# Kernel optimization log

Measured on AMD Instinct MI355X. Metric: run time of the kernel, lower is better.

The kernel has to match this reference:

```python
import jax, jax.numpy as jnp
import numpy as np

N, E, B, D, H, L = 50000, 800000, 16, 64, 128, 2


def _lin(h, w, b):
    return h @ w + b


def _scatter_mean(v, idx, n):
    s = jax.ops.segment_sum(v, idx, num_segments=n)
    c = jax.ops.segment_sum(jnp.ones((v.shape[0],), v.dtype), idx, num_segments=n)
    return s / jnp.maximum(c, 1.0)[:, None]


def setup_inputs() -> dict:
    key = jax.random.key(0)
    ks = iter(jax.random.split(key, 40))

    def p(*shape):
        return jax.random.normal(next(ks), shape, dtype=jnp.float32) * 0.05

    inp = {
        "x": jax.random.normal(next(ks), (N, D), dtype=jnp.float32),
        "edge_attr": jax.random.normal(next(ks), (E, D), dtype=jnp.float32),
        "u": jax.random.normal(next(ks), (B, D), dtype=jnp.float32),
        "e_w1": p(L, 4 * D, H), "e_b1": p(L, H),
        "e_w2": p(L, H, H), "e_b2": p(L, H),
        "e_w3": p(L, H, D), "e_b3": p(L, D),
        "n1_w1": p(L, 2 * D, H), "n1_b1": p(L, H),
        "n1_w2": p(L, H, H), "n1_b2": p(L, H),
        "n2_w1": p(L, D + H + D, H), "n2_b1": p(L, H),
        "n2_w2": p(L, H, D), "n2_b2": p(L, D),
        "g_w1": p(L, 3 * D, H), "g_b1": p(L, H),
        "g_w2": p(L, H, D), "g_b2": p(L, D),
        "edge_index": jax.random.randint(next(ks), (2, E), 0, N, dtype=jnp.int32),
        "batch": jnp.sort(jax.random.randint(next(ks), (N,), 0, B, dtype=jnp.int32)),
    }
    return inp


def _forward(x, edge_attr, u, params, edge_index, batch):
    row, col = edge_index[0], edge_index[1]
    eb = batch[row]  # [E] graph id per edge
    x0, e0, u0 = x, edge_attr, u
    for l in range(L):
        (e_w1, e_b1, e_w2, e_b2, e_w3, e_b3,
         n1_w1, n1_b1, n1_w2, n1_b2,
         n2_w1, n2_b1, n2_w2, n2_b2,
         g_w1, g_b1, g_w2, g_b2) = [pm[l] for pm in params]
        # Edge model: [E, e+2n+u] -> MLP -> [E, D]
        h = jnp.concatenate([x[row], x[col], edge_attr, u[eb]], axis=1)
        h = jax.nn.relu(_lin(h, e_w1, e_b1))
        h = jax.nn.relu(_lin(h, e_w2, e_b2))
        edge_attr = _lin(h, e_w3, e_b3)
        # Node model: gather src node + edge, MLP1, scatter_mean onto dest, MLP2
        se = jnp.concatenate([x[row], edge_attr], axis=1)  # [E, 2D]
        se = _lin(jax.nn.relu(_lin(se, n1_w1, n1_b1)), n1_w2, n1_b2)
        agg = _scatter_mean(se, col, N)  # [N, H]
        xh = jnp.concatenate([x, agg, u[batch]], axis=1)
        x = _lin(jax.nn.relu(_lin(xh, n2_w1, n2_b1)), n2_w2, n2_b2)
        # Global model: per-graph means of updated nodes/edges
        e_agg = _scatter_mean(edge_attr, eb, B)
        n_agg = _scatter_mean(x, batch, B)
        uh = jnp.concatenate([u, n_agg, e_agg], axis=1)
        u = _lin(jax.nn.relu(_lin(uh, g_w1, g_b1)), g_w2, g_b2)
    return x + x0, edge_attr + e0, u + u0


def reference(x, edge_attr, u, e_w1, e_b1, e_w2, e_b2, e_w3, e_b3, n1_w1, n1_b1, n1_w2, n1_b2, n2_w1, n2_b1, n2_w2, n2_b2, g_w1, g_b1, g_w2, g_b2, edge_index, batch):
    params = (e_w1, e_b1, e_w2, e_b2, e_w3, e_b3,
              n1_w1, n1_b1, n1_w2, n1_b2,
              n2_w1, n2_b1, n2_w2, n2_b2,
              g_w1, g_b1, g_w2, g_b2)
    return _forward(x, edge_attr, u, params, edge_index, batch)
```

## Files before the change

kernel.cpp:

```cpp
#include <hip/hip_runtime.h>

#define N_NODES 50000
#define E_EDGES 800000
#define NG 16
#define DD 64
#define HH 128
#define NB_SCAN 49

typedef __attribute__((ext_vector_type(8))) __bf16 bf16x8;
typedef __attribute__((ext_vector_type(4))) float f32x4;
typedef unsigned int uint;
typedef unsigned short ushort;
typedef __attribute__((ext_vector_type(4))) uint uint4v;

#define MFMA16(a,b,c) __builtin_amdgcn_mfma_f32_16x16x32_bf16((a),(b),(c),0,0,0)

__device__ __forceinline__ ushort f2bf(float f){
  uint u = __builtin_bit_cast(uint, f);
  u += 0x7fffu + ((u >> 16) & 1u);
  return (ushort)(u >> 16);
}
__device__ __forceinline__ uint pk2(float a, float b){
  return (uint)f2bf(a) | ((uint)f2bf(b) << 16);
}
__device__ __forceinline__ float bflo(uint u){ return __builtin_bit_cast(float, u << 16); }
__device__ __forceinline__ float bfhi(uint u){ return __builtin_bit_cast(float, u & 0xffff0000u); }

__device__ __forceinline__ bf16x8 ldfrag(const char* base, int row, int byteoff){
  uint4v v = *(const uint4v*)(base + row*256 + (byteoff ^ ((row & 7) << 4)));
  return __builtin_bit_cast(bf16x8, v);
}
__device__ __forceinline__ uint4v ld_chunk(const char* base, int row, int c16){
  return *(const uint4v*)(base + row*256 + ((c16*16) ^ ((row & 7) << 4)));
}
__device__ __forceinline__ void st_h(char* base, int row, int col, float v){
  *(ushort*)(base + row*256 + ((col*2) ^ ((row & 7) << 4))) = f2bf(v);
}
__device__ __forceinline__ void st_chunk(char* base, int row, int c16, uint4v v){
  *(uint4v*)(base + row*256 + ((c16*16) ^ ((row & 7) << 4))) = v;
}
__device__ __forceinline__ void pack16(char* dst, int r, int c16, const float* src){
  float4 lo = *(const float4*)src;
  float4 hi = *(const float4*)(src + 4);
  uint4v v; v.x = pk2(lo.x, lo.y); v.y = pk2(lo.z, lo.w);
  v.z = pk2(hi.x, hi.y); v.w = pk2(hi.z, hi.w);
  st_chunk(dst, r, c16, v);
}

__device__ __forceinline__ void stage_b(char* sB, const ushort* wt,
                                        int Nout, int Ktot, int koff, int t, int stride){
  for (int task = t; task < Nout*16; task += stride){
    int n = task >> 4, c = task & 15;
    uint4v v = *(const uint4v*)(wt + (long)n*Ktot + koff + c*8);
    st_chunk(sB, n, c, v);
  }
}

__device__ __forceinline__ void gemmN4(const char* A, const char* B,
                                       int mw, int nh, int l15, int lhi, f32x4* acc){
  #pragma unroll
  for (int kt = 0; kt < 4; ++kt){
    bf16x8 a = ldfrag(A, mw*16 + l15, kt*64 + lhi*16);
    #pragma unroll
    for (int n = 0; n < 4; ++n){
      bf16x8 bb = ldfrag(B, (nh*4 + n)*16 + l15, kt*64 + lhi*16);
      acc[n] = MFMA16(a, bb, acc[n]);
    }
  }
}
template<bool RELU>
__device__ __forceinline__ void epiN4(char* dst, const f32x4* acc, const float* bias,
                                      int mw, int nh, int l15, int lhi){
  #pragma unroll
  for (int n = 0; n < 4; ++n){
    int col = nh*64 + n*16 + l15;
    float bv = bias[col];
    #pragma unroll
    for (int j = 0; j < 4; ++j){
      int r = mw*16 + lhi*4 + j;
      float v = acc[n][j] + bv;
      if (RELU) v = fmaxf(v, 0.f);
      st_h(dst, r, col, v);
    }
  }
}

template<int NT>
__device__ __forceinline__ void gemm_acc(const char* A, const char* B,
                                         int wv, int l15, int lhi, f32x4* acc){
  #pragma unroll
  for (int kt = 0; kt < 4; ++kt){
    bf16x8 a = ldfrag(A, wv*16 + l15, kt*64 + lhi*16);
    #pragma unroll
    for (int n = 0; n < NT; ++n){
      bf16x8 bb = ldfrag(B, n*16 + l15, kt*64 + lhi*16);
      acc[n] = MFMA16(a, bb, acc[n]);
    }
  }
}
template<int NT, bool RELU>
__device__ __forceinline__ void epi_lds(char* dst, const f32x4* acc, const float* bias,
                                        int wv, int l15, int lhi){
  #pragma unroll
  for (int n = 0; n < NT; ++n){
    float bv = bias[n*16 + l15];
    #pragma unroll
    for (int j = 0; j < 4; ++j){
      int r = wv*16 + lhi*4 + j;
      float v = acc[n][j] + bv;
      if (RELU) v = fmaxf(v, 0.f);
      st_h(dst, r, n*16 + l15, v);
    }
  }
}

__global__ void pack_weights(const float* __restrict__ e1, const float* __restrict__ e2,
                             const float* __restrict__ e3, const float* __restrict__ n11,
                             const float* __restrict__ n12, const float* __restrict__ n21,
                             const float* __restrict__ n22, ushort* __restrict__ out){
  int idx = blockIdx.x * 256 + threadIdx.x;
  int l = idx / 131072, r = idx % 131072;
  const float* src; int K, N, off;
  if      (r <  32768){ src = e1;  K = 256; N = 128; off = 0; }
  else if (r <  49152){ src = e2;  K = 128; N = 128; off = 32768; }
  else if (r <  57344){ src = e3;  K = 128; N = 64;  off = 49152; }
  else if (r <  73728){ src = n11; K = 128; N = 128; off = 57344; }
  else if (r <  90112){ src = n12; K = 128; N = 128; off = 73728; }
  else if (r < 122880){ src = n21; K = 256; N = 128; off = 90112; }
  else                { src = n22; K = 128; N = 64;  off = 122880; }
  int q = r - off; int k = q / N; int n = q % N;
  out[(long)l*131072 + off + n*K + k] = f2bf(src[(long)l*K*N + q]);
}

__global__ void hist_kernel(const int* __restrict__ edge_index, const int* __restrict__ batch,
                            int* __restrict__ deg, float* __restrict__ cnt_eb){
  __shared__ float h[NG];
  int t = threadIdx.x;
  if (t < NG) h[t] = 0.f;
  __syncthreads();
  int e = blockIdx.x * 256 + t;
  if (e < E_EDGES){
    atomicAdd(deg + edge_index[E_EDGES + e], 1);
    atomicAdd(&h[batch[edge_index[e]]], 1.f);
  }
  __syncthreads();
  if (t < NG) atomicAdd(cnt_eb + t, h[t]);
}
__global__ void count_nodes_kernel(const int* __restrict__ batch, float* __restrict__ cnt_b){
  __shared__ float h[NG];
  int t = threadIdx.x;
  if (t < NG) h[t] = 0.f;
  __syncthreads();
  int n = blockIdx.x * 256 + t;
  if (n < N_NODES) atomicAdd(&h[batch[n]], 1.f);
  __syncthreads();
  if (t < NG) atomicAdd(cnt_b + t, h[t]);
}
__global__ void scan_a(const int* __restrict__ deg, int* __restrict__ bsum){
  __shared__ int red[1024];
  int i = blockIdx.x*1024 + threadIdx.x;
  red[threadIdx.x] = (i < N_NODES) ? deg[i] : 0;
  __syncthreads();
  for (int s = 512; s > 0; s >>= 1){
    if ((int)threadIdx.x < s) red[threadIdx.x] += red[threadIdx.x + s];
    __syncthreads();
  }
  if (threadIdx.x == 0) bsum[blockIdx.x] = red[0];
}
__global__ void scan_b(const int* __restrict__ bsum, int* __restrict__ bbase){
  if (threadIdx.x == 0){
    int run = 0;
    for (int b = 0; b < NB_SCAN; ++b){ int v = bsum[b]; bbase[b] = run; run += v; }
  }
}
__global__ void scan_c(const int* __restrict__ deg, const int* __restrict__ bbase,
                       int* __restrict__ off, int* __restrict__ cursor){
  __shared__ int sc[1024];
  int i = blockIdx.x*1024 + threadIdx.x;
  int v = (i < N_NODES) ? deg[i] : 0;
  sc[threadIdx.x] = v;
  __syncthreads();
  for (int d = 1; d < 1024; d <<= 1){
    int add = ((int)threadIdx.x >= d) ? sc[threadIdx.x - d] : 0;
    __syncthreads();
    sc[threadIdx.x] += add;
    __syncthreads();
  }
  if (i < N_NODES){
    int ex = sc[threadIdx.x] - v + bbase[blockIdx.x];
    off[i] = ex; cursor[i] = ex;
  }
}
__global__ void fill_kernel(const int* __restrict__ edge_index, int* __restrict__ cursor,
                            int* __restrict__ pos){
  int e = blockIdx.x*256 + threadIdx.x;
  if (e < E_EDGES){
    int c = edge_index[E_EDGES + e];
    pos[e] = atomicAdd(&cursor[c], 1);
  }
}

template<bool CSR>
__global__ __launch_bounds__(512, 4) void edge_kernel(
    const float* __restrict__ x_cur, const float* __restrict__ e_cur,
    const float* __restrict__ u_cur, const float* __restrict__ e_resid,
    const int* __restrict__ edge_index, const int* __restrict__ batch,
    const int* __restrict__ pos_arr,
    const ushort* __restrict__ w_e1, const ushort* __restrict__ w_e2,
    const ushort* __restrict__ w_e3, const ushort* __restrict__ w_n11,
    const ushort* __restrict__ w_n12,
    const float* __restrict__ b_e1, const float* __restrict__ b_e2,
    const float* __restrict__ b_e3, const float* __restrict__ b_n11,
    const float* __restrict__ b_n12,
    float* __restrict__ e_out, ushort* __restrict__ se_buf,
    float* __restrict__ agg_sum, float* __restrict__ e_agg, int has_resid)
{
  __shared__ __align__(16) char sA[16384];
  __shared__ __align__(16) char sB[32768];
  __shared__ __align__(16) char sH[16384];
  __shared__ int sRow[64], sCol[64], sEb[64];
  __shared__ float sEagg[NG*DD];

  const int t = threadIdx.x;
  const int wv = t >> 6, ln = t & 63, l15 = ln & 15, lhi = ln >> 4;
  const int mw = wv & 3, nh = wv >> 2;
  const int ebase = blockIdx.x * 64;

  if (t < 64){
    int r = edge_index[ebase + t];
    sRow[t] = r; sCol[t] = edge_index[E_EDGES + ebase + t]; sEb[t] = batch[r];
  }
  for (int i = t; i < NG*DD; i += 512) sEagg[i] = 0.f;
  __syncthreads();

  f32x4 acc1[4];
  #pragma unroll
  for (int n = 0; n < 4; ++n) acc1[n] = f32x4{0.f,0.f,0.f,0.f};
  for (int kh = 0; kh < 2; ++kh){
    for (int task = t; task < 1024; task += 512){
      int r = task >> 4, c = task & 15;
      const float* src;
      if (kh == 0) src = (c < 8) ? (x_cur + (long)sRow[r]*DD + c*8)
                                 : (x_cur + (long)sCol[r]*DD + (c-8)*8);
      else         src = (c < 8) ? (e_cur + (long)(ebase + r)*DD + c*8)
                                 : (u_cur + (long)sEb[r]*DD + (c-8)*8);
      pack16(sA, r, c, src);
    }
    stage_b(sB, w_e1, 128, 256, kh*128, t, 512);
    __syncthreads();
    gemmN4(sA, sB, mw, nh, l15, lhi, acc1);
    __syncthreads();
  }
  epiN4<true>(sH, acc1, b_e1, mw, nh, l15, lhi);
  stage_b(sB, w_e2, 128, 128, 0, t, 512);
  __syncthreads();

  f32x4 acc2[4];
  #pragma unroll
  for (int n = 0; n < 4; ++n) acc2[n] = f32x4{0.f,0.f,0.f,0.f};
  gemmN4(sH, sB, mw, nh, l15, lhi, acc2);
  __syncthreads();
  epiN4<true>(sA, acc2, b_e2, mw, nh, l15, lhi);
  stage_b(sB, w_e3, 64, 128, 0, t, 512);
  __syncthreads();

  f32x4 acc3[2];
  acc3[0] = f32x4{0.f,0.f,0.f,0.f}; acc3[1] = f32x4{0.f,0.f,0.f,0.f};
  #pragma unroll
  for (int kt = 0; kt < 4; ++kt){
    bf16x8 a = ldfrag(sA, mw*16 + l15, kt*64 + lhi*16);
    #pragma unroll
    for (int n = 0; n < 2; ++n){
      bf16x8 bb = ldfrag(sB, (nh*2 + n)*16 + l15, kt*64 + lhi*16);
      acc3[n] = MFMA16(a, bb, acc3[n]);
    }
  }
  float enew[2][4];
  #pragma unroll
  for (int n = 0; n < 2; ++n){
    int col = nh*32 + n*16 + l15;
    float bv = b_e3[col];
    #pragma unroll
    for (int j = 0; j < 4; ++j){
      int r = mw*16 + lhi*4 + j;
      float v = acc3[n][j] + bv;
      enew[n][j] = v;
      long eg = (long)(ebase + r)*DD + col;
      e_out[eg] = has_resid ? (v + e_resid[eg]) : v;
      atomicAdd(&sEagg[sEb[r]*DD + col], v);
    }
  }
  __syncthreads();

  #pragma unroll
  for (int n = 0; n < 2; ++n){
    #pragma unroll
    for (int j = 0; j < 4; ++j){
      int r = mw*16 + lhi*4 + j;
      st_h(sA, r, 64 + nh*32 + n*16 + l15, enew[n][j]);
    }
  }
  { int r = t >> 3, c = t & 7;
    pack16(sA, r, c, x_cur + (long)sRow[r]*DD + c*8); }
  stage_b(sB, w_n11, 128, 128, 0, t, 512);
  __syncthreads();

  f32x4 acc4[4];
  #pragma unroll
  for (int n = 0; n < 4; ++n) acc4[n] = f32x4{0.f,0.f,0.f,0.f};
  gemmN4(sA, sB, mw, nh, l15, lhi, acc4);
  __syncthreads();
  epiN4<true>(sH, acc4, b_n11, mw, nh, l15, lhi);
  stage_b(sB, w_n12, 128, 128, 0, t, 512);
  __syncthreads();

  f32x4 acc5[4];
  #pragma unroll
  for (int n = 0; n < 4; ++n) acc5[n] = f32x4{0.f,0.f,0.f,0.f};
  gemmN4(sH, sB, mw, nh, l15, lhi, acc5);

  if (CSR){
    epiN4<false>(sA, acc5, b_n12, mw, nh, l15, lhi);
    __syncthreads();
    int r = t >> 3, oct = t & 7;
    long p = pos_arr[ebase + r];
    uint4v v0 = ld_chunk(sA, r, oct*2);
    uint4v v1 = ld_chunk(sA, r, oct*2 + 1);
    *(uint4v*)(se_buf + p*128 + oct*16) = v0;
    *(uint4v*)(se_buf + p*128 + oct*16 + 8) = v1;
  } else {
    #pragma unroll
    for (int n = 0; n < 4; ++n){
      int col = nh*64 + n*16 + l15;
      float bv = b_n12[col];
      #pragma unroll
      for (int j = 0; j < 4; ++j){
        int r = mw*16 + lhi*4 + j;
        atomicAdd(agg_sum + (long)sCol[r]*HH + col, acc5[n][j] + bv);
      }
    }
  }
  for (int i = t; i < NG*DD; i += 512) atomicAdd(e_agg + i, sEagg[i]);
}

template<bool CSR>
__global__ __launch_bounds__(256, 2) void node_kernel(
    const float* __restrict__ x_cur, const float* __restrict__ u_cur,
    const float* __restrict__ x_resid, const int* __restrict__ batch,
    const ushort* __restrict__ se_buf, const int* __restrict__ deg,
    const int* __restrict__ off, const float* __restrict__ agg_sum,
    const ushort* __restrict__ w_n21, const ushort* __restrict__ w_n22,
    const float* __restrict__ b_n21, const float* __restrict__ b_n22,
    float* __restrict__ x_out, float* __restrict__ n_agg, int has_resid)
{
  __shared__ __align__(16) char sA[16384];
  __shared__ __align__(16) char sB[32768];
  __shared__ __align__(16) char sH[16384];
  __shared__ int sBat[64], sDeg[64], sOff[64];
  __shared__ float sRinv[64];
  __shared__ float sNagg[NG*DD];

  const int t = threadIdx.x;
  const int wv = t >> 6, ln = t & 63, l15 = ln & 15, lhi = ln >> 4;
  const int n0 = blockIdx.x * 64;

  if (t < 64){
    int nd = n0 + t;
    int ok = nd < N_NODES;
    sBat[t] = ok ? batch[nd] : 0;
    int d = ok ? deg[nd] : 0;
    sDeg[t] = d;
    sOff[t] = ok ? off[nd] : 0;
    sRinv[t] = 1.f / fmaxf((float)d, 1.f);
  }
  for (int i = t; i < NG*DD; i += 256) sNagg[i] = 0.f;
  __syncthreads();

  float s[32];
  const int r4 = t >> 2, q = t & 3;
  if (CSR){
    #pragma unroll
    for (int k = 0; k < 32; ++k) s[k] = 0.f;
    int d = sDeg[r4], o = sOff[r4];
    for (int i = 0; i < d; ++i){
      const ushort* src = se_buf + (long)(o + i)*HH + q*32;
      #pragma unroll
      for (int c = 0; c < 4; ++c){
        uint4v v = *(const uint4v*)(src + c*8);
        #pragma unroll
        for (int jj = 0; jj < 4; ++jj){
          s[c*8 + jj*2]     += bflo(v[jj]);
          s[c*8 + jj*2 + 1] += bfhi(v[jj]);
        }
      }
    }
    float riv = sRinv[r4];
    #pragma unroll
    for (int k = 0; k < 32; ++k) s[k] *= riv;
  }

  f32x4 acc[8];
  #pragma unroll
  for (int n = 0; n < 8; ++n) acc[n] = f32x4{0.f,0.f,0.f,0.f};

  for (int half = 0; half < 2; ++half){
    if (CSR){
      for (int task = t; task < 512; task += 256){
        int r = task >> 3, c = task & 7;
        int nd = n0 + r;
        bool ok = nd < N_NODES;
        float4 lo = {0,0,0,0}, hi = {0,0,0,0};
        if (ok){
          const float* src = (half == 0) ? (x_cur + (long)nd*DD + c*8)
                                         : (u_cur + (long)sBat[r]*DD + c*8);
          lo = *(const float4*)src; hi = *(const float4*)(src + 4);
        }
        uint4v v; v.x = pk2(lo.x, lo.y); v.y = pk2(lo.z, lo.w);
        v.z = pk2(hi.x, hi.y); v.w = pk2(hi.z, hi.w);
        st_chunk(sA, r, (half == 0) ? c : (8 + c), v);
      }
      if ((half == 0 && q < 2) || (half == 1 && q >= 2)){
        int cbase = (half == 0) ? (8 + q*4) : ((q - 2)*4);
        #pragma unroll
        for (int cc = 0; cc < 4; ++cc){
          uint4v v;
          v.x = pk2(s[cc*8+0], s[cc*8+1]); v.y = pk2(s[cc*8+2], s[cc*8+3]);
          v.z = pk2(s[cc*8+4], s[cc*8+5]); v.w = pk2(s[cc*8+6], s[cc*8+7]);
          st_chunk(sA, r4, cbase + cc, v);
        }
      }
    } else {
      for (int task = t; task < 1024; task += 256){
        int r = task >> 4, c = task & 15;
        int nd = n0 + r;
        bool ok = nd < N_NODES;
        float scale = 1.f;
        const float* src;
        if (half == 0){
          if (c < 8) src = x_cur + (long)nd*DD + c*8;
          else { src = agg_sum + (long)nd*HH + (c-8)*8; scale = sRinv[r]; }
        } else {
          if (c < 8){ src = agg_sum + (long)nd*HH + 64 + c*8; scale = sRinv[r]; }
          else src = u_cur + (long)sBat[r]*DD + (c-8)*8;
        }
        float4 lo = {0,0,0,0}, hi = {0,0,0,0};
        if (ok){ lo = *(const float4*)src; hi = *(const float4*)(src + 4); }
        uint4v v; v.x = pk2(lo.x*scale, lo.y*scale); v.y = pk2(lo.z*scale, lo.w*scale);
        v.z = pk2(hi.x*scale, hi.y*scale); v.w = pk2(hi.z*scale, hi.w*scale);
        st_chunk(sA, r, c, v);
      }
    }
    stage_b(sB, w_n21, 128, 256, half*128, t, 256);
    __syncthreads();
    gemm_acc<8>(sA, sB, wv, l15, lhi, acc);
    __syncthreads();
  }
  epi_lds<8, true>(sH, acc, b_n21, wv, l15, lhi);
  stage_b(sB, w_n22, 64, 128, 0, t, 256);
  __syncthreads();

  f32x4 acc2[4];
  #pragma unroll
  for (int n = 0; n < 4; ++n) acc2[n] = f32x4{0.f,0.f,0.f,0.f};
  gemm_acc<4>(sH, sB, wv, l15, lhi, acc2);

  #pragma unroll
  for (int n = 0; n < 4; ++n){
    float bv = b_n22[n*16 + l15];
    #pragma unroll
    for (int j = 0; j < 4; ++j){
      int r = wv*16 + lhi*4 + j;
      int nd = n0 + r;
      if (nd < N_NODES){
        int col = n*16 + l15;
        float v = acc2[n][j] + bv;
        long xg = (long)nd*DD + col;
        x_out[xg] = has_resid ? (v + x_resid[xg]) : v;
        atomicAdd(&sNagg[sBat[r]*DD + col], v);
      }
    }
  }
  __syncthreads();
  for (int i = t; i < NG*DD; i += 256) atomicAdd(n_agg + i, sNagg[i]);
}

__global__ void global_kernel(const float* __restrict__ u_cur, const float* __restrict__ n_agg,
                              const float* __restrict__ e_agg, const float* __restrict__ cnt_b,
                              const float* __restrict__ cnt_e,
                              const float* __restrict__ g_w1, const float* __restrict__ g_b1,
                              const float* __restrict__ g_w2, const float* __restrict__ g_b2,
                              const float* __restrict__ u_resid, float* __restrict__ u_out,
                              int has_resid)
{
  int g = blockIdx.x, t = threadIdx.x;
  __shared__ float uh[192];
  __shared__ float hb[128];
  float v;
  if (t < 64)       v = u_cur[g*64 + t];
  else if (t < 128) v = n_agg[g*64 + (t-64)] / fmaxf(cnt_b[g], 1.f);
  else              v = e_agg[g*64 + (t-128)] / fmaxf(cnt_e[g], 1.f);
  uh[t] = v;
  __syncthreads();
  if (t < 128){
    float s = g_b1[t];
    for (int k = 0; k < 192; ++k) s += uh[k] * g_w1[k*128 + t];
    hb[t] = fmaxf(s, 0.f);
  }
  __syncthreads();
  if (t < 64){
    float s = g_b2[t];
    for (int k = 0; k < 128; ++k) s += hb[k] * g_w2[k*64 + t];
    if (has_resid) s += u_resid[g*64 + t];
    u_out[g*64 + t] = s;
  }
}

extern "C" void kernel_launch(void* const* d_in, const int* in_sizes, int n_in,
                              void* d_out, int out_size, void* d_ws, size_t ws_size,
                              hipStream_t stream)
{
  const float* x0   = (const float*)d_in[0];
  const float* e0   = (const float*)d_in[1];
  const float* u0   = (const float*)d_in[2];
  const float* e_w1 = (const float*)d_in[3];
  const float* e_b1 = (const float*)d_in[4];
  const float* e_w2 = (const float*)d_in[5];
  const float* e_b2 = (const float*)d_in[6];
  const float* e_w3 = (const float*)d_in[7];
  const float* e_b3 = (const float*)d_in[8];
  const float* n1_w1 = (const float*)d_in[9];
  const float* n1_b1 = (const float*)d_in[10];
  const float* n1_w2 = (const float*)d_in[11];
  const float* n1_b2 = (const float*)d_in[12];
  const float* n2_w1 = (const float*)d_in[13];
  const float* n2_b1 = (const float*)d_in[14];
  const float* n2_w2 = (const float*)d_in[15];
  const float* n2_b2 = (const float*)d_in[16];
  const float* g_w1 = (const float*)d_in[17];
  const float* g_b1 = (const float*)d_in[18];
  const float* g_w2 = (const float*)d_in[19];
  const float* g_b2 = (const float*)d_in[20];
  const int* edge_index = (const int*)d_in[21];
  const int* batch      = (const int*)d_in[22];

  float* out_x = (float*)d_out;
  float* out_e = out_x + (long)N_NODES*DD;
  float* out_u = out_e + (long)E_EDGES*DD;

  char* ws = (char*)d_ws;
  int*   deg    = (int*)(ws + 0);
  int*   off    = (int*)(ws + 200000);
  int*   cursor = (int*)(ws + 400000);
  int*   bsum   = (int*)(ws + 600000);
  int*   bbase  = (int*)(ws + 600256);
  float* cnt_eb = (float*)(ws + 600512);
  float* cnt_b  = (float*)(ws + 600576);
  float* e_agg  = (float*)(ws + 600640);
  float* n_agg  = (float*)(ws + 604736);
  ushort* packed = (ushort*)(ws + 608832);
  const size_t big = 1133120;
  bool use_csr = ws_size >= (size_t)(big + 204800000 + 3200000);
  ushort* se_buf = (ushort*)(ws + big);
  int*    pos    = (int*)(ws + big + 204800000);
  float*  agg_sum = (float*)(ws + big);

  (void)hipMemsetAsync(deg, 0, 200000, stream);
  (void)hipMemsetAsync(cnt_eb, 0, 128, stream);
  pack_weights<<<1024, 256, 0, stream>>>(e_w1, e_w2, e_w3, n1_w1, n1_w2, n2_w1, n2_w2, packed);
  hist_kernel<<<3125, 256, 0, stream>>>(edge_index, batch, deg, cnt_eb);
  count_nodes_kernel<<<196, 256, 0, stream>>>(batch, cnt_b);
  if (use_csr){
    scan_a<<<NB_SCAN, 1024, 0, stream>>>(deg, bsum);
    scan_b<<<1, 64, 0, stream>>>(bsum, bbase);
    scan_c<<<NB_SCAN, 1024, 0, stream>>>(deg, bbase, off, cursor);
    fill_kernel<<<3125, 256, 0, stream>>>(edge_index, cursor, pos);
  }

  const float* xc = x0;
  const float* ec = e0;
  const float* uc = u0;
  for (int l = 0; l < 2; ++l){
    (void)hipMemsetAsync(e_agg, 0, 8192, stream);
    if (!use_csr)
      (void)hipMemsetAsync(agg_sum, 0, (size_t)N_NODES*HH*4, stream);
    const ushort* P = packed + (long)l*131072;
    if (use_csr){
      edge_kernel<true><<<E_EDGES/64, 512, 0, stream>>>(
          xc, ec, uc, e0, edge_index, batch, pos,
          P + 0, P + 32768, P + 49152, P + 57344, P + 73728,
          e_b1 + l*128, e_b2 + l*128, e_b3 + l*64, n1_b1 + l*128, n1_b2 + l*128,
          out_e, se_buf, agg_sum, e_agg, l == 1);
      node_kernel<true><<<782, 256, 0, stream>>>(
          xc, uc, x0, batch, se_buf, deg, off, agg_sum,
          P + 90112, P + 122880, n2_b1 + l*128, n2_b2 + l*64,
          out_x, n_agg, l == 1);
    } else {
      edge_kernel<false><<<E_EDGES/64, 512, 0, stream>>>(
          xc, ec, uc, e0, edge_index, batch, pos,
          P + 0, P + 32768, P + 49152, P + 57344, P + 73728,
          e_b1 + l*128, e_b2 + l*128, e_b3 + l*64, n1_b1 + l*128, n1_b2 + l*128,
          out_e, se_buf, agg_sum, e_agg, l == 1);
      node_kernel<false><<<782, 256, 0, stream>>>(
          xc, uc, x0, batch, se_buf, deg, off, agg_sum,
          P + 90112, P + 122880, n2_b1 + l*128, n2_b2 + l*64,
          out_x, n_agg, l == 1);
    }
    global_kernel<<<NG, 192, 0, stream>>>(
        uc, n_agg, e_agg, cnt_b, cnt_eb,
        g_w1 + l*192*128, g_b1 + l*128, g_w2 + l*128*64, g_b2 + l*64,
        u0, out_u, l == 1);
    xc = out_x; ec = out_e; uc = out_u;
  }
}
```

Measured before the change: 1.805 ms.

## Split edge kernel in two and fold edge output layer into node MLP

The single fused edge kernel becomes two kernels. k123 computes the first two edge-MLP layers for 128-edge tiles and writes the bf16 hidden state into the edge output buffer as scratch. k45 then computes the edge output (layer 3) and the node-MLP first layer in parallel from that hidden state. This works because a precomputed combined weight W3·W1_bottom plus a folded bias removes the serial dependency on layer 3's output. The intent is fewer dependent GEMM stages and better MFMA tiling with 2x8 accumulator blocks per wave. The cost is an extra global write and read of a 128-wide bf16 hidden tensor per layer, and different bf16 rounding from the composed weights.

```diff
diff --git a/kernel.cpp b/kernel.cpp
--- a/kernel.cpp
+++ b/kernel.cpp
@@ -39,6 +39,29 @@
 __device__ __forceinline__ void st_chunk(char* base, int row, int c16, uint4v v){
   *(uint4v*)(base + row*256 + ((c16*16) ^ ((row & 7) << 4))) = v;
 }
+__device__ __forceinline__ bf16x8 ldfrag128(const char* base, int row, int byteoff){
+  uint4v v = *(const uint4v*)(base + row*128 + (byteoff ^ ((row & 7) << 4)));
+  return __builtin_bit_cast(bf16x8, v);
+}
+__device__ __forceinline__ void st_chunk128(char* base, int row, int c16, uint4v v){
+  *(uint4v*)(base + row*128 + ((c16*16) ^ ((row & 7) << 4))) = v;
+}
+__device__ __forceinline__ void pack16_128(char* dst, int r, int c16, const float* src){
+  float4 lo = *(const float4*)src;
+  float4 hi = *(const float4*)(src + 4);
+  uint4v v; v.x = pk2(lo.x, lo.y); v.y = pk2(lo.z, lo.w);
+  v.z = pk2(hi.x, hi.y); v.w = pk2(hi.z, hi.w);
+  st_chunk128(dst, r, c16, v);
+}
+
+__device__ __forceinline__ void stage_b(char* sB, const ushort* wt,
+                                        int Nout, int Ktot, int koff, int t, int stride){
+  for (int task = t; task < Nout*16; task += stride){
+    int n = task >> 4, c = task & 15;
+    uint4v v = *(const uint4v*)(wt + (long)n*Ktot + koff + c*8);
+    st_chunk(sB, n, c, v);
+  }
+}
 __device__ __forceinline__ void pack16(char* dst, int r, int c16, const float* src){
   float4 lo = *(const float4*)src;
   float4 hi = *(const float4*)(src + 4);
@@ -46,45 +69,6 @@
   v.z = pk2(hi.x, hi.y); v.w = pk2(hi.z, hi.w);
   st_chunk(dst, r, c16, v);
 }
-
-__device__ __forceinline__ void stage_b(char* sB, const ushort* wt,
-                                        int Nout, int Ktot, int koff, int t, int stride){
-  for (int task = t; task < Nout*16; task += stride){
-    int n = task >> 4, c = task & 15;
-    uint4v v = *(const uint4v*)(wt + (long)n*Ktot + koff + c*8);
-    st_chunk(sB, n, c, v);
-  }
-}
-
-__device__ __forceinline__ void gemmN4(const char* A, const char* B,
-                                       int mw, int nh, int l15, int lhi, f32x4* acc){
-  #pragma unroll
-  for (int kt = 0; kt < 4; ++kt){
-    bf16x8 a = ldfrag(A, mw*16 + l15, kt*64 + lhi*16);
-    #pragma unroll
-    for (int n = 0; n < 4; ++n){
-      bf16x8 bb = ldfrag(B, (nh*4 + n)*16 + l15, kt*64 + lhi*16);
-      acc[n] = MFMA16(a, bb, acc[n]);
-    }
-  }
-}
-template<bool RELU>
-__device__ __forceinline__ void epiN4(char* dst, const f32x4* acc, const float* bias,
-                                      int mw, int nh, int l15, int lhi){
-  #pragma unroll
-  for (int n = 0; n < 4; ++n){
-    int col = nh*64 + n*16 + l15;
-    float bv = bias[col];
-    #pragma unroll
-    for (int j = 0; j < 4; ++j){
-      int r = mw*16 + lhi*4 + j;
-      float v = acc[n][j] + bv;
-      if (RELU) v = fmaxf(v, 0.f);
-      st_h(dst, r, col, v);
-    }
-  }
-}
-
 template<int NT>
 __device__ __forceinline__ void gemm_acc(const char* A, const char* B,
                                          int wv, int l15, int lhi, f32x4* acc){
@@ -115,21 +99,44 @@
 }
 
 __global__ void pack_weights(const float* __restrict__ e1, const float* __restrict__ e2,
-                             const float* __restrict__ e3, const float* __restrict__ n11,
-                             const float* __restrict__ n12, const float* __restrict__ n21,
-                             const float* __restrict__ n22, ushort* __restrict__ out){
+                             const float* __restrict__ e3, const float* __restrict__ n12,
+                             const float* __restrict__ n21, const float* __restrict__ n22,
+                             ushort* __restrict__ out){
   int idx = blockIdx.x * 256 + threadIdx.x;
-  int l = idx / 131072, r = idx % 131072;
+  int l = idx / 114688, r = idx % 114688;
   const float* src; int K, N, off;
   if      (r <  32768){ src = e1;  K = 256; N = 128; off = 0; }
   else if (r <  49152){ src = e2;  K = 128; N = 128; off = 32768; }
   else if (r <  57344){ src = e3;  K = 128; N = 64;  off = 49152; }
-  else if (r <  73728){ src = n11; K = 128; N = 128; off = 57344; }
-  else if (r <  90112){ src = n12; K = 128; N = 128; off = 73728; }
-  else if (r < 122880){ src = n21; K = 256; N = 128; off = 90112; }
-  else                { src = n22; K = 128; N = 64;  off = 122880; }
+  else if (r <  73728){ src = n12; K = 128; N = 128; off = 57344; }
+  else if (r < 106496){ src = n21; K = 256; N = 128; off = 73728; }
+  else                { src = n22; K = 128; N = 64;  off = 106496; }
   int q = r - off; int k = q / N; int n = q % N;
-  out[(long)l*131072 + off + n*K + k] = f2bf(src[(long)l*K*N + q]);
+  out[(long)l*139264 + off + n*K + k] = f2bf(src[(long)l*K*N + q]);
+}
+
+__global__ void make_wc(const float* __restrict__ n1w1, const float* __restrict__ ew3,
+                        const float* __restrict__ n1b1, const float* __restrict__ eb3,
+                        ushort* __restrict__ packed, float* __restrict__ biasc){
+  int l = blockIdx.x, t = threadIdx.x;
+  const float* W1 = n1w1 + (long)l*128*128;
+  const float* W3 = ew3 + (long)l*128*64;
+  ushort* wc = packed + (long)l*139264 + 114688;
+  for (int i = t; i < 8192; i += 256){
+    int k = i >> 7, n = i & 127;
+    wc[n*192 + k] = f2bf(W1[k*128 + n]);
+  }
+  for (int i = t; i < 16384; i += 256){
+    int k2 = i >> 7, n = i & 127;
+    float s = 0.f;
+    for (int m = 0; m < 64; ++m) s += W3[k2*64 + m] * W1[(64 + m)*128 + n];
+    wc[n*192 + 64 + k2] = f2bf(s);
+  }
+  if (t < 128){
+    float s = n1b1[l*128 + t];
+    for (int m = 0; m < 64; ++m) s += eb3[l*64 + m] * W1[(64 + m)*128 + t];
+    biasc[l*128 + t] = s;
+  }
 }
 
 __global__ void hist_kernel(const int* __restrict__ edge_index, const int* __restrict__ batch,
@@ -200,147 +207,307 @@
   }
 }
 
+__global__ __launch_bounds__(256, 3) void k123_kernel(
+    const float* __restrict__ x_cur, const float* e_cur,
+    const float* __restrict__ u_cur,
+    const int* __restrict__ ei, const int* __restrict__ batch,
+    const ushort* __restrict__ w1t, const ushort* __restrict__ w2t,
+    const float* __restrict__ be1, const float* __restrict__ be2,
+    ushort* h2g)
+{
+  __shared__ __align__(16) char lds[49152];
+  __shared__ int sRow[128], sCol[128], sEb[128];
+  char* A  = lds;
+  char* B  = lds + 16384;
+  char* OV = lds + 16384;
+  const int t = threadIdx.x;
+  const int wv = t >> 6, l15 = t & 15, lhi = (t >> 4) & 3;
+  const int ebase = blockIdx.x * 128;
+
+  if (t < 128){
+    int r = ei[ebase + t];
+    sRow[t] = r; sCol[t] = ei[E_EDGES + ebase + t]; sEb[t] = batch[r];
+  }
+  __syncthreads();
+
+  f32x4 acc[2][8];
+  #pragma unroll
+  for (int m = 0; m < 2; ++m)
+    #pragma unroll
+    for (int n = 0; n < 8; ++n) acc[m][n] = f32x4{0,0,0,0};
+
+  for (int c = 0; c < 4; ++c){
+    #pragma unroll
+    for (int it = 0; it < 4; ++it){
+      int task = t + it*256, r = task >> 3, c16 = task & 7;
+      const float* s;
+      if      (c == 0) s = x_cur + (long)sRow[r]*DD + c16*8;
+      else if (c == 1) s = x_cur + (long)sCol[r]*DD + c16*8;
+      else if (c == 2) s = e_cur + (long)(ebase + r)*DD + c16*8;
+      else             s = u_cur + (long)sEb[r]*DD + c16*8;
+      pack16_128(A, r, c16, s);
+    }
+    #pragma unroll
+    for (int it = 0; it < 4; ++it){
+      int task = t + it*256, n = task >> 3, c16 = task & 7;
+      st_chunk128(B, n, c16, *(const uint4v*)(w1t + (long)n*256 + c*64 + c16*8));
+    }
+    __syncthreads();
+    #pragma unroll
+    for (int kt = 0; kt < 2; ++kt){
+      bf16x8 a0 = ldfrag128(A, wv*32 + l15,      kt*64 + lhi*16);
+      bf16x8 a1 = ldfrag128(A, wv*32 + 16 + l15, kt*64 + lhi*16);
+      #pragma unroll
+      for (int n = 0; n < 8; ++n){
+        bf16x8 bb = ldfrag128(B, n*16 + l15, kt*64 + lhi*16);
+        acc[0][n] = MFMA16(a0, bb, acc[0][n]);
+        acc[1][n] = MFMA16(a1, bb, acc[1][n]);
+      }
+    }
+    __syncthreads();
+  }
+  #pragma unroll
+  for (int m = 0; m < 2; ++m)
+    #pragma unroll
+    for (int n = 0; n < 8; ++n){
+      int col = n*16 + l15;
+      float bv = be1[col];
+      #pragma unroll
+      for (int j = 0; j < 4; ++j)
+        st_h(OV, wv*32 + m*16 + lhi*4 + j, col, fmaxf(acc[m][n][j] + bv, 0.f));
+    }
+  __syncthreads();
+
+  #pragma unroll
+  for (int m = 0; m < 2; ++m)
+    #pragma unroll
+    for (int n = 0; n < 8; ++n) acc[m][n] = f32x4{0,0,0,0};
+  for (int kc = 0; kc < 2; ++kc){
+    #pragma unroll
+    for (int it = 0; it < 4; ++it){
+      int task = t + it*256, n = task >> 3, c16 = task & 7;
+      st_chunk128(A, n, c16, *(const uint4v*)(w2t + (long)n*128 + kc*64 + c16*8));
+    }
+    __syncthreads();
+    #pragma unroll
+    for (int kt = 0; kt < 2; ++kt){
+      bf16x8 a0 = ldfrag(OV, wv*32 + l15,      kc*128 + kt*64 + lhi*16);
+      bf16x8 a1 = ldfrag(OV, wv*32 + 16 + l15, kc*128 + kt*64 + lhi*16);
+      #pragma unroll
+      for (int n = 0; n < 8; ++n){
+        bf16x8 bb = ldfrag128(A, n*16 + l15, kt*64 + lhi*16);
+        acc[0][n] = MFMA16(a0, bb, acc[0][n]);
+        acc[1][n] = MFMA16(a1, bb, acc[1][n]);
+      }
+    }
+    __syncthreads();
+  }
+  #pragma unroll
+  for (int m = 0; m < 2; ++m)
+    #pragma unroll
+    for (int n = 0; n < 8; ++n){
+      int col = n*16 + l15;
+      float bv = be2[col];
+      #pragma unroll
+      for (int j = 0; j < 4; ++j)
+        st_h(OV, wv*32 + m*16 + lhi*4 + j, col, fmaxf(acc[m][n][j] + bv, 0.f));
+    }
+  __syncthreads();
+  #pragma unroll
+  for (int it = 0; it < 8; ++it){
+    int task = t + it*256, r = task >> 4, c16 = task & 15;
+    *(uint4v*)(h2g + (long)(ebase + r)*HH + c16*8) = ld_chunk(OV, r, c16);
+  }
+}
+
 template<bool CSR>
-__global__ __launch_bounds__(512, 4) void edge_kernel(
-    const float* __restrict__ x_cur, const float* __restrict__ e_cur,
-    const float* __restrict__ u_cur, const float* __restrict__ e_resid,
-    const int* __restrict__ edge_index, const int* __restrict__ batch,
+__global__ __launch_bounds__(256, 3) void k45_kernel(
+    const float* __restrict__ x_cur, const ushort* h2g,
+    const int* __restrict__ ei, const int* __restrict__ batch,
     const int* __restrict__ pos_arr,
-    const ushort* __restrict__ w_e1, const ushort* __restrict__ w_e2,
-    const ushort* __restrict__ w_e3, const ushort* __restrict__ w_n11,
-    const ushort* __restrict__ w_n12,
-    const float* __restrict__ b_e1, const float* __restrict__ b_e2,
-    const float* __restrict__ b_e3, const float* __restrict__ b_n11,
-    const float* __restrict__ b_n12,
-    float* __restrict__ e_out, ushort* __restrict__ se_buf,
-    float* __restrict__ agg_sum, float* __restrict__ e_agg, int has_resid)
+    const ushort* __restrict__ w3t, const ushort* __restrict__ wct,
+    const ushort* __restrict__ w5t,
+    const float* __restrict__ be3, const float* __restrict__ biasc,
+    const float* __restrict__ bn12,
+    float* e_outf, const float* __restrict__ e_resid,
+    ushort* __restrict__ se_buf, float* __restrict__ agg_sum,
+    float* __restrict__ e_agg, int has_resid)
 {
-  __shared__ __align__(16) char sA[16384];
-  __shared__ __align__(16) char sB[32768];
-  __shared__ __align__(16) char sH[16384];
-  __shared__ int sRow[64], sCol[64], sEb[64];
+  __shared__ __align__(16) char lds[49152];
   __shared__ float sEagg[NG*DD];
-
+  __shared__ int sIdx[128];
+  char* A  = lds;
+  char* B  = lds + 16384;
+  char* B2 = lds + 32768;
+  char* OV = lds + 16384;
   const int t = threadIdx.x;
-  const int wv = t >> 6, ln = t & 63, l15 = ln & 15, lhi = ln >> 4;
-  const int mw = wv & 3, nh = wv >> 2;
-  const int ebase = blockIdx.x * 64;
-
-  if (t < 64){
-    int r = edge_index[ebase + t];
-    sRow[t] = r; sCol[t] = edge_index[E_EDGES + ebase + t]; sEb[t] = batch[r];
-  }
-  for (int i = t; i < NG*DD; i += 512) sEagg[i] = 0.f;
-  __syncthreads();
-
-  f32x4 acc1[4];
-  #pragma unroll
-  for (int n = 0; n < 4; ++n) acc1[n] = f32x4{0.f,0.f,0.f,0.f};
-  for (int kh = 0; kh < 2; ++kh){
-    for (int task = t; task < 1024; task += 512){
-      int r = task >> 4, c = task & 15;
-      const float* src;
-      if (kh == 0) src = (c < 8) ? (x_cur + (long)sRow[r]*DD + c*8)
-                                 : (x_cur + (long)sCol[r]*DD + (c-8)*8);
-      else         src = (c < 8) ? (e_cur + (long)(ebase + r)*DD + c*8)
-                                 : (u_cur + (long)sEb[r]*DD + (c-8)*8);
-      pack16(sA, r, c, src);
-    }
-    stage_b(sB, w_e1, 128, 256, kh*128, t, 512);
-    __syncthreads();
-    gemmN4(sA, sB, mw, nh, l15, lhi, acc1);
-    __syncthreads();
-  }
-  epiN4<true>(sH, acc1, b_e1, mw, nh, l15, lhi);
-  stage_b(sB, w_e2, 128, 128, 0, t, 512);
-  __syncthreads();
-
-  f32x4 acc2[4];
-  #pragma unroll
-  for (int n = 0; n < 4; ++n) acc2[n] = f32x4{0.f,0.f,0.f,0.f};
-  gemmN4(sH, sB, mw, nh, l15, lhi, acc2);
-  __syncthreads();
-  epiN4<true>(sA, acc2, b_e2, mw, nh, l15, lhi);
-  stage_b(sB, w_e3, 64, 128, 0, t, 512);
-  __syncthreads();
-
-  f32x4 acc3[2];
-  acc3[0] = f32x4{0.f,0.f,0.f,0.f}; acc3[1] = f32x4{0.f,0.f,0.f,0.f};
-  #pragma unroll
-  for (int kt = 0; kt < 4; ++kt){
-    bf16x8 a = ldfrag(sA, mw*16 + l15, kt*64 + lhi*16);
-    #pragma unroll
-    for (int n = 0; n < 2; ++n){
-      bf16x8 bb = ldfrag(sB, (nh*2 + n)*16 + l15, kt*64 + lhi*16);
-      acc3[n] = MFMA16(a, bb, acc3[n]);
-    }
-  }
-  float enew[2][4];
-  #pragma unroll
-  for (int n = 0; n < 2; ++n){
-    int col = nh*32 + n*16 + l15;
-    float bv = b_e3[col];
-    #pragma unroll
-    for (int j = 0; j < 4; ++j){
-      int r = mw*16 + lhi*4 + j;
-      float v = acc3[n][j] + bv;
-      enew[n][j] = v;
-      long eg = (long)(ebase + r)*DD + col;
-      e_out[eg] = has_resid ? (v + e_resid[eg]) : v;
-      atomicAdd(&sEagg[sEb[r]*DD + col], v);
-    }
-  }
-  __syncthreads();
-
-  #pragma unroll
-  for (int n = 0; n < 2; ++n){
-    #pragma unroll
-    for (int j = 0; j < 4; ++j){
-      int r = mw*16 + lhi*4 + j;
-      st_h(sA, r, 64 + nh*32 + n*16 + l15, enew[n][j]);
-    }
-  }
-  { int r = t >> 3, c = t & 7;
-    pack16(sA, r, c, x_cur + (long)sRow[r]*DD + c*8); }
-  stage_b(sB, w_n11, 128, 128, 0, t, 512);
-  __syncthreads();
-
-  f32x4 acc4[4];
-  #pragma unroll
-  for (int n = 0; n < 4; ++n) acc4[n] = f32x4{0.f,0.f,0.f,0.f};
-  gemmN4(sA, sB, mw, nh, l15, lhi, acc4);
-  __syncthreads();
-  epiN4<true>(sH, acc4, b_n11, mw, nh, l15, lhi);
-  stage_b(sB, w_n12, 128, 128, 0, t, 512);
-  __syncthreads();
-
-  f32x4 acc5[4];
-  #pragma unroll
-  for (int n = 0; n < 4; ++n) acc5[n] = f32x4{0.f,0.f,0.f,0.f};
-  gemmN4(sH, sB, mw, nh, l15, lhi, acc5);
+  const int wv = t >> 6, l15 = t & 15, lhi = (t >> 4) & 3;
+  const int ebase = blockIdx.x * 128;
+
+  if (t < 128) sIdx[t] = ei[ebase + t];
+  for (int i = t; i < NG*DD; i += 256) sEagg[i] = 0.f;
+  __syncthreads();
+
+  f32x4 acc4[2][8], acc3[2][4];
+  #pragma unroll
+  for (int m = 0; m < 2; ++m){
+    #pragma unroll
+    for (int n = 0; n < 8; ++n) acc4[m][n] = f32x4{0,0,0,0};
+    #pragma unroll
+    for (int n = 0; n < 4; ++n) acc3[m][n] = f32x4{0,0,0,0};
+  }
+
+  for (int c = 0; c < 3; ++c){
+    if (c == 0){
+      #pragma unroll
+      for (int it = 0; it < 4; ++it){
+        int task = t + it*256, r = task >> 3, c16 = task & 7;
+        pack16_128(A, r, c16, x_cur + (long)sIdx[r]*DD + c16*8);
+      }
+      #pragma unroll
+      for (int it = 0; it < 4; ++it){
+        int task = t + it*256, n = task >> 4, c16 = task & 15;
+        st_chunk(B2, n, c16, *(const uint4v*)(w3t + (long)n*128 + c16*8));
+      }
+    } else {
+      #pragma unroll
+      for (int it = 0; it < 4; ++it){
+        int task = t + it*256, r = task >> 3, c16 = task & 7;
+        st_chunk128(A, r, c16,
+            *(const uint4v*)(h2g + (long)(ebase + r)*HH + (c-1)*64 + c16*8));
+      }
+    }
+    #pragma unroll
+    for (int it = 0; it < 4; ++it){
+      int task = t + it*256, n = task >> 3, c16 = task & 7;
+      st_chunk128(B, n, c16, *(const uint4v*)(wct + (long)n*192 + c*64 + c16*8));
+    }
+    __syncthreads();
+    #pragma unroll
+    for (int kt = 0; kt < 2; ++kt){
+      bf16x8 a0 = ldfrag128(A, wv*32 + l15,      kt*64 + lhi*16);
+      bf16x8 a1 = ldfrag128(A, wv*32 + 16 + l15, kt*64 + lhi*16);
+      #pragma unroll
+      for (int n = 0; n < 8; ++n){
+        bf16x8 bb = ldfrag128(B, n*16 + l15, kt*64 + lhi*16);
+        acc4[0][n] = MFMA16(a0, bb, acc4[0][n]);
+        acc4[1][n] = MFMA16(a1, bb, acc4[1][n]);
+      }
+      if (c >= 1){
+        #pragma unroll
+        for (int n = 0; n < 4; ++n){
+          bf16x8 b2 = ldfrag(B2, n*16 + l15, (c-1)*128 + kt*64 + lhi*16);
+          acc3[0][n] = MFMA16(a0, b2, acc3[0][n]);
+          acc3[1][n] = MFMA16(a1, b2, acc3[1][n]);
+        }
+      }
+    }
+    __syncthreads();
+  }
+
+  #pragma unroll
+  for (int m = 0; m < 2; ++m)
+    #pragma unroll
+    for (int n = 0; n < 4; ++n){
+      int col = n*16 + l15;
+      float bv = be3[col];
+      #pragma unroll
+      for (int j = 0; j < 4; ++j){
+        int row = wv*32 + m*16 + lhi*4 + j;
+        float v = acc3[m][n][j] + bv;
+        long eg = (long)(ebase + row)*DD + col;
+        e_outf[eg] = has_resid ? (v + e_resid[eg]) : v;
+        int eb = batch[ei[ebase + row]];
+        atomicAdd(&sEagg[eb*DD + col], v);
+      }
+    }
+  #pragma unroll
+  for (int m = 0; m < 2; ++m)
+    #pragma unroll
+    for (int n = 0; n < 8; ++n){
+      int col = n*16 + l15;
+      float bv = biasc[col];
+      #pragma unroll
+      for (int j = 0; j < 4; ++j)
+        st_h(OV, wv*32 + m*16 + lhi*4 + j, col, fmaxf(acc4[m][n][j] + bv, 0.f));
+    }
+  #pragma unroll
+  for (int it = 0; it < 4; ++it){
+    int task = t + it*256, n = task >> 3, c16 = task & 7;
+    st_chunk128(A, n, c16, *(const uint4v*)(w5t + (long)n*128 + c16*8));
+  }
+  if (t < 128) sIdx[t] = CSR ? pos_arr[ebase + t] : ei[E_EDGES + ebase + t];
+  __syncthreads();
+
+  f32x4 acc5[2][8];
+  #pragma unroll
+  for (int m = 0; m < 2; ++m)
+    #pragma unroll
+    for (int n = 0; n < 8; ++n) acc5[m][n] = f32x4{0,0,0,0};
+  #pragma unroll
+  for (int kt = 0; kt < 2; ++kt){
+    bf16x8 a0 = ldfrag(OV, wv*32 + l15,      kt*64 + lhi*16);
+    bf16x8 a1 = ldfrag(OV, wv*32 + 16 + l15, kt*64 + lhi*16);
+    #pragma unroll
+    for (int n = 0; n < 8; ++n){
+      bf16x8 bb = ldfrag128(A, n*16 + l15, kt*64 + lhi*16);
+      acc5[0][n] = MFMA16(a0, bb, acc5[0][n]);
+      acc5[1][n] = MFMA16(a1, bb, acc5[1][n]);
+    }
+  }
+  __syncthreads();
+  #pragma unroll
+  for (int it = 0; it < 4; ++it){
+    int task = t + it*256, n = task >> 3, c16 = task & 7;
+    st_chunk128(A, n, c16, *(const uint4v*)(w5t + (long)n*128 + 64 + c16*8));
+  }
+  __syncthreads();
+  #pragma unroll
+  for (int kt = 0; kt < 2; ++kt){
+    bf16x8 a0 = ldfrag(OV, wv*32 + l15,      128 + kt*64 + lhi*16);
+    bf16x8 a1 = ldfrag(OV, wv*32 + 16 + l15, 128 + kt*64 + lhi*16);
+    #pragma unroll
+    for (int n = 0; n < 8; ++n){
+      bf16x8 bb = ldfrag128(A, n*16 + l15, kt*64 + lhi*16);
+      acc5[0][n] = MFMA16(a0, bb, acc5[0][n]);
+      acc5[1][n] = MFMA16(a1, bb, acc5[1][n]);
+    }
+  }
+  __syncthreads();
 
   if (CSR){
-    epiN4<false>(sA, acc5, b_n12, mw, nh, l15, lhi);
-    __syncthreads();
-    int r = t >> 3, oct = t & 7;
-    long p = pos_arr[ebase + r];
-    uint4v v0 = ld_chunk(sA, r, oct*2);
-    uint4v v1 = ld_chunk(sA, r, oct*2 + 1);
-    *(uint4v*)(se_buf + p*128 + oct*16) = v0;
-    *(uint4v*)(se_buf + p*128 + oct*16 + 8) = v1;
+    #pragma unroll
+    for (int m = 0; m < 2; ++m)
+      #pragma unroll
+      for (int n = 0; n < 8; ++n){
+        int col = n*16 + l15;
+        float bv = bn12[col];
+        #pragma unroll
+        for (int j = 0; j < 4; ++j)
+          st_h(OV, wv*32 + m*16 + lhi*4 + j, col, acc5[m][n][j] + bv);
+      }
+    __syncthreads();
+    #pragma unroll
+    for (int it = 0; it < 8; ++it){
+      int task = t + it*256, r = task >> 4, c16 = task & 15;
+      *(uint4v*)(se_buf + (long)sIdx[r]*HH + c16*8) = ld_chunk(OV, r, c16);
+    }
   } else {
     #pragma unroll
-    for (int n = 0; n < 4; ++n){
-      int col = nh*64 + n*16 + l15;
-      float bv = b_n12[col];
-      #pragma unroll
-      for (int j = 0; j < 4; ++j){
-        int r = mw*16 + lhi*4 + j;
-        atomicAdd(agg_sum + (long)sCol[r]*HH + col, acc5[n][j] + bv);
-      }
-    }
-  }
-  for (int i = t; i < NG*DD; i += 512) atomicAdd(e_agg + i, sEagg[i]);
+    for (int m = 0; m < 2; ++m)
+      #pragma unroll
+      for (int n = 0; n < 8; ++n){
+        int col = n*16 + l15;
+        float bv = bn12[col];
+        #pragma unroll
+        for (int j = 0; j < 4; ++j){
+          int row = wv*32 + m*16 + lhi*4 + j;
+          atomicAdd(agg_sum + (long)sIdx[row]*HH + col, acc5[m][n][j] + bv);
+        }
+      }
+    __syncthreads();
+  }
+  for (int i = t; i < NG*DD; i += 256) atomicAdd(e_agg + i, sEagg[i]);
 }
 
 template<bool CSR>
@@ -557,8 +724,9 @@
   float* cnt_b  = (float*)(ws + 600576);
   float* e_agg  = (float*)(ws + 600640);
   float* n_agg  = (float*)(ws + 604736);
-  ushort* packed = (ushort*)(ws + 608832);
-  const size_t big = 1133120;
+  float* biascf = (float*)(ws + 608832);
+  ushort* packed = (ushort*)(ws + 609856);
+  const size_t big = 1166912;
   bool use_csr = ws_size >= (size_t)(big + 204800000 + 3200000);
   ushort* se_buf = (ushort*)(ws + big);
   int*    pos    = (int*)(ws + big + 204800000);
@@ -566,7 +734,8 @@
 
   (void)hipMemsetAsync(deg, 0, 200000, stream);
   (void)hipMemsetAsync(cnt_eb, 0, 128, stream);
-  pack_weights<<<1024, 256, 0, stream>>>(e_w1, e_w2, e_w3, n1_w1, n1_w2, n2_w1, n2_w2, packed);
+  pack_weights<<<896, 256, 0, stream>>>(e_w1, e_w2, e_w3, n1_w2, n2_w1, n2_w2, packed);
+  make_wc<<<2, 256, 0, stream>>>(n1_w1, e_w3, n1_b1, e_b3, packed, biascf);
   hist_kernel<<<3125, 256, 0, stream>>>(edge_index, batch, deg, cnt_eb);
   count_nodes_kernel<<<196, 256, 0, stream>>>(batch, cnt_b);
   if (use_csr){
@@ -583,26 +752,30 @@
     (void)hipMemsetAsync(e_agg, 0, 8192, stream);
     if (!use_csr)
       (void)hipMemsetAsync(agg_sum, 0, (size_t)N_NODES*HH*4, stream);
-    const ushort* P = packed + (long)l*131072;
+    const ushort* P = packed + (long)l*139264;
+    k123_kernel<<<6250, 256, 0, stream>>>(
+        xc, ec, uc, edge_index, batch,
+        P + 0, P + 32768, e_b1 + l*128, e_b2 + l*128,
+        (ushort*)out_e);
     if (use_csr){
-      edge_kernel<true><<<E_EDGES/64, 512, 0, stream>>>(
-          xc, ec, uc, e0, edge_index, batch, pos,
-          P + 0, P + 32768, P + 49152, P + 57344, P + 73728,
-          e_b1 + l*128, e_b2 + l*128, e_b3 + l*64, n1_b1 + l*128, n1_b2 + l*128,
-          out_e, se_buf, agg_sum, e_agg, l == 1);
+      k45_kernel<true><<<6250, 256, 0, stream>>>(
+          xc, (const ushort*)out_e, edge_index, batch, pos,
+          P + 49152, P + 114688, P + 57344,
+          e_b3 + l*64, biascf + l*128, n1_b2 + l*128,
+          out_e, e0, se_buf, agg_sum, e_agg, l == 1);
       node_kernel<true><<<782, 256, 0, stream>>>(
           xc, uc, x0, batch, se_buf, deg, off, agg_sum,
-          P + 90112, P + 122880, n2_b1 + l*128, n2_b2 + l*64,
+          P + 73728, P + 106496, n2_b1 + l*128, n2_b2 + l*64,
           out_x, n_agg, l == 1);
     } else {
-      edge_kernel<false><<<E_EDGES/64, 512, 0, stream>>>(
-          xc, ec, uc, e0, edge_index, batch, pos,
-          P + 0, P + 32768, P + 49152, P + 57344, P + 73728,
-          e_b1 + l*128, e_b2 + l*128, e_b3 + l*64, n1_b1 + l*128, n1_b2 + l*128,
-          out_e, se_buf, agg_sum, e_agg, l == 1);
+      k45_kernel<false><<<6250, 256, 0, stream>>>(
+          xc, (const ushort*)out_e, edge_index, batch, pos,
+          P + 49152, P + 114688, P + 57344,
+          e_b3 + l*64, biascf + l*128, n1_b2 + l*128,
+          out_e, e0, se_buf, agg_sum, e_agg, l == 1);
       node_kernel<false><<<782, 256, 0, stream>>>(
           xc, uc, x0, batch, se_buf, deg, off, agg_sum,
-          P + 90112, P + 122880, n2_b1 + l*128, n2_b2 + l*64,
+          P + 73728, P + 106496, n2_b1 + l*128, n2_b2 + l*64,
           out_x, n_agg, l == 1);
     }
     global_kernel<<<NG, 192, 0, stream>>>(
```

After: 1.910 ms. 5.9% more time.
